# Kernel optimization log

Measured on AMD Instinct MI355X. Metric: run time of the kernel, lower is better.

## Reference

```python
import jax, jax.numpy as jnp
import numpy as np

DIM = 1024
NUM_HEADS = 16
HEAD_DIM = 64
SEQ_LEN = 4096
RMS_EPS = 1e-6


def rotary_tables(T, head_dim):
    # modded-nanogpt style rotary: frequencies only on first half of the half-dim,
    # second half zeroed (identity rotation).
    angular_freq = (1.0 / 1024.0) ** jnp.linspace(0.0, 1.0, head_dim // 4)
    angular_freq = jnp.concatenate([angular_freq, jnp.zeros(head_dim // 4)])
    t = jnp.arange(T, dtype=jnp.float32)
    theta = t[:, None] * angular_freq[None, :]  # [T, D/2]
    return jnp.cos(theta), jnp.sin(theta)


def apply_rotary(x, cos, sin):
    # x: [B, T, H, D]
    xf = x.astype(jnp.float32)
    x1, x2 = jnp.split(xf, 2, axis=-1)
    c = cos[None, :, None, :]
    s = sin[None, :, None, :]
    y1 = x1 * c + x2 * s
    y2 = x1 * (-s) + x2 * c
    return jnp.concatenate([y1, y2], axis=-1).astype(x.dtype)


def rms_norm(x):
    return x * jax.lax.rsqrt(jnp.mean(x * x, axis=-1, keepdims=True) + RMS_EPS)


def setup_inputs() -> dict:
    key = jax.random.key(0)
    k1, k2, k3 = jax.random.split(key, 3)
    hdim = NUM_HEADS * HEAD_DIM
    std = 0.5 * DIM ** (-0.5)
    bound = (3.0 ** 0.5) * std
    x = jax.random.normal(k1, (1, SEQ_LEN, DIM), dtype=jnp.float32)
    qkv_w = jax.random.uniform(k2, (3 * hdim, DIM), minval=-bound, maxval=bound, dtype=jnp.float32)
    # original zero-inits c_proj; use small random weights for a nontrivial baseline
    proj_w = jax.random.normal(k3, (DIM, hdim), dtype=jnp.float32) * 0.02
    lambdas = jnp.array([0.5], dtype=jnp.float32)
    return {"x": x, "qkv_w": qkv_w, "lambdas": lambdas, "proj_w": proj_w}


def reference(x, qkv_w, lambdas, proj_w):
    B, T, _ = x.shape
    H, D = NUM_HEADS, HEAD_DIM
    scale = 1.0 / (D ** 0.5)
    qkv = jnp.einsum('btc,fc->btf', x, qkv_w)            # [B, T, 3*H*D]
    qkv = qkv.reshape(B, T, 3 * H, D)
    q, k, v = jnp.split(qkv, 3, axis=-2)                  # each [B, T, H, D]
    q, k = rms_norm(q), rms_norm(k)
    cos, sin = rotary_tables(T, D)
    q, k = apply_rotary(q, cos, sin), apply_rotary(k, cos, sin)
    v = lambdas[0] * v
    scores = jnp.einsum('bqhd,bkhd->bhqk', q, k) * scale  # [B, H, T, T]
    causal = jnp.tril(jnp.ones((T, T), dtype=bool))
    scores = jnp.where(causal[None, None], scores, -jnp.inf)
    p = jax.nn.softmax(scores, axis=-1)
    y = jnp.einsum('bhqk,bkhd->bqhd', p, v)               # [B, T, H, D]
    y = y.reshape(B, T, H * D)
    return jnp.einsum('btf,cf->btc', y, proj_w)           # [B, T, DIM]
```

## Files before the change

### kernel.cpp

```cpp
#include <hip/hip_runtime.h>
#include <stdint.h>

#define SEQ 4096
#define NHEAD 16
#define HDIM 64

typedef __attribute__((ext_vector_type(4))) float f32x4;
typedef __attribute__((ext_vector_type(16))) float f32x16;
typedef __attribute__((ext_vector_type(8))) __bf16 bf16x8;
typedef __attribute__((ext_vector_type(8))) unsigned short u16x8;
typedef __attribute__((ext_vector_type(4))) unsigned short u16x4;
typedef __attribute__((ext_vector_type(4))) unsigned int u32x4;

static __device__ __forceinline__ float bf2f(unsigned short u) {
    unsigned int x = ((unsigned int)u) << 16;
    return __builtin_bit_cast(float, x);
}
static __device__ __forceinline__ unsigned short f2bf(float f) {
    unsigned int u = __builtin_bit_cast(unsigned int, f);
    u += 0x7FFFu + ((u >> 16) & 1u);
    return (unsigned short)(u >> 16);
}
static __device__ __forceinline__ f32x4 mfma_bf16_16x16x32(u16x8 a, u16x8 b, f32x4 c) {
    return __builtin_amdgcn_mfma_f32_16x16x32_bf16(
        __builtin_bit_cast(bf16x8, a), __builtin_bit_cast(bf16x8, b), c, 0, 0, 0);
}
static __device__ __forceinline__ f32x16 mfma_bf16_32x32x16(u16x8 a, u16x8 b, f32x16 c) {
    return __builtin_amdgcn_mfma_f32_32x32x16_bf16(
        __builtin_bit_cast(bf16x8, a), __builtin_bit_cast(bf16x8, b), c, 0, 0, 0);
}
static __device__ __forceinline__ void gload_lds16(const void* g, void* l) {
    __builtin_amdgcn_global_load_lds(
        (__attribute__((address_space(1))) unsigned int*)g,
        (__attribute__((address_space(3))) unsigned int*)l,
        16, 0, 0);
}
static __device__ __forceinline__ unsigned int cvtpk_bf16(float lo, float hi) {
    unsigned int r;
    asm("v_cvt_pk_bf16_f32 %0, %1, %2" : "=v"(r) : "v"(lo), "v"(hi));
    return r;
}

__global__ void cvt3_kernel(const float* __restrict__ s0, unsigned short* __restrict__ d0, int n0q,
                            const float* __restrict__ s1, unsigned short* __restrict__ d1, int n1q,
                            const float* __restrict__ s2, unsigned short* __restrict__ d2, int n2q)
{
    const int stride = gridDim.x * blockDim.x;
    const int total = n0q + n1q + n2q;
    for (int i = blockIdx.x * blockDim.x + threadIdx.x; i < total; i += stride) {
        const float* src; unsigned short* dst; int j;
        if (i < n0q)            { src = s0; dst = d0; j = i; }
        else if (i < n0q + n1q) { src = s1; dst = d1; j = i - n0q; }
        else                    { src = s2; dst = d2; j = i - n0q - n1q; }
        f32x4 v = *(const f32x4*)(src + (size_t)j * 4);
        u16x4 o;
#pragma unroll
        for (int k = 0; k < 4; k++) o[k] = f2bf(v[k]);
        *(u16x4*)(dst + (size_t)j * 4) = o;
    }
}

template<int OUT_BF16>
__global__ __launch_bounds__(256) void gemm_bt_kernel(
    const unsigned short* __restrict__ A,
    const unsigned short* __restrict__ B,
    void* __restrict__ Cv,
    int M, int N, int K, int lda)
{
    __shared__ __align__(16) unsigned short As[128 * 64];
    __shared__ __align__(16) unsigned short Bs[128 * 64];
    const int tid = threadIdx.x;
    const int lane = tid & 63;
    const int wave = tid >> 6;
    const int wm = (wave >> 1) * 64;
    const int wn = (wave & 1) * 64;
    const int bm = blockIdx.y * 128, bn = blockIdx.x * 128;
    const int l15 = lane & 15, l4 = lane >> 4;

    f32x4 acc[4][4];
#pragma unroll
    for (int i = 0; i < 4; i++)
#pragma unroll
        for (int j = 0; j < 4; j++) acc[i][j] = (f32x4){0.f, 0.f, 0.f, 0.f};

    const int srow = tid >> 3;
    const int scol = (tid & 7) * 8;
    const unsigned short* Ab = A + (size_t)(bm + srow) * lda + scol;
    const unsigned short* Bb = B + (size_t)(bn + srow) * K + scol;

    for (int kt = 0; kt < K; kt += 64) {
#pragma unroll
        for (int ci = 0; ci < 4; ci++)
            gload_lds16(Ab + (size_t)ci * 32 * lda + kt, &As[ci * 2048 + tid * 8]);
#pragma unroll
        for (int ci = 0; ci < 4; ci++)
            gload_lds16(Bb + (size_t)ci * 32 * K + kt, &Bs[ci * 2048 + tid * 8]);
        __syncthreads();
#pragma unroll
        for (int ks = 0; ks < 2; ks++) {
            const int kc = ks * 32 + l4 * 8;
            u16x8 af[4], bfr[4];
#pragma unroll
            for (int i = 0; i < 4; i++)
                af[i] = *(const u16x8*)&As[(wm + i * 16 + l15) * 64 + kc];
#pragma unroll
            for (int j = 0; j < 4; j++)
                bfr[j] = *(const u16x8*)&Bs[(wn + j * 16 + l15) * 64 + kc];
#pragma unroll
            for (int i = 0; i < 4; i++)
#pragma unroll
                for (int j = 0; j < 4; j++)
                    acc[i][j] = mfma_bf16_16x16x32(af[i], bfr[j], acc[i][j]);
        }
        __syncthreads();
    }

    const int orow = bm + wm + l4 * 4;
    const int ocol = bn + wn + l15;
#pragma unroll
    for (int i = 0; i < 4; i++)
#pragma unroll
        for (int j = 0; j < 4; j++)
#pragma unroll
            for (int r = 0; r < 4; r++) {
                size_t idx = (size_t)(orow + i * 16 + r) * N + (ocol + j * 16);
                if (OUT_BF16) ((unsigned short*)Cv)[idx] = f2bf(acc[i][j][r]);
                else          ((float*)Cv)[idx] = acc[i][j][r];
            }
}

__global__ __launch_bounds__(256) void rope_norm_kernel(
    const unsigned short* __restrict__ qkv,
    const float* __restrict__ lambdas,
    unsigned short* __restrict__ qh,
    unsigned short* __restrict__ kh,
    unsigned short* __restrict__ vh)
{
    const int lane = threadIdx.x & 63;
    const int wave = threadIdx.x >> 6;
    const int vec = blockIdx.x * 4 + wave;
    const int t = vec >> 4;
    const int h = vec & 15;
    const size_t base = (size_t)t * 3072 + h * 64 + lane;
    float q = bf2f(qkv[base]);
    float k = bf2f(qkv[base + 1024]);
    float v = bf2f(qkv[base + 2048]);
    float sq = q * q, sk = k * k;
#pragma unroll
    for (int m = 1; m < 64; m <<= 1) {
        sq += __shfl_xor(sq, m);
        sk += __shfl_xor(sk, m);
    }
    q *= rsqrtf(sq * (1.0f / 64.0f) + 1e-6f);
    k *= rsqrtf(sk * (1.0f / 64.0f) + 1e-6f);
    const int i = lane & 31;
    float w = (i < 16) ? exp2f(-(10.0f / 15.0f) * (float)i) : 0.0f;
    float th = (float)t * w;
    float c = cosf(th), s = sinf(th);
    float qp = __shfl_xor(q, 32);
    float kp = __shfl_xor(k, 32);
    float sg = (lane < 32) ? s : -s;
    float qo = (q * c + qp * sg) * 0.1803368801111244f;
    float ko = k * c + kp * sg;
    float vo = v * lambdas[0];
    const size_t o = ((size_t)h * SEQ + t) * 64 + lane;
    qh[o] = f2bf(qo);
    kh[o] = f2bf(ko);
    vh[o] = f2bf(vo);
}

__global__ __launch_bounds__(256) void transpose_v_kernel(
    const unsigned short* __restrict__ vh, unsigned short* __restrict__ vT)
{
    __shared__ __align__(16) unsigned short tile[64][72];
    const int h = blockIdx.x >> 6;
    const int tt = (blockIdx.x & 63) * 64;
    const int tid = threadIdx.x;
    const int row = tid >> 2;
    const int c0 = (tid & 3) * 16;
    const u16x8* src = (const u16x8*)(vh + ((size_t)h * SEQ + tt + row) * 64 + c0);
    u16x8 a = src[0], b = src[1];
#pragma unroll
    for (int j = 0; j < 8; j++) { tile[row][c0 + j] = a[j]; tile[row][c0 + 8 + j] = b[j]; }
    __syncthreads();
    u16x8 o0, o1;
#pragma unroll
    for (int j = 0; j < 8; j++) { o0[j] = tile[c0 + j][row]; o1[j] = tile[c0 + 8 + j][row]; }
    u16x8* dst = (u16x8*)(vT + ((size_t)h * 64 + row) * SEQ + tt + c0);
    dst[0] = o0; dst[1] = o1;
}

__global__ __launch_bounds__(256, 3) void attn_kernel(
    const unsigned short* __restrict__ qh,
    const unsigned short* __restrict__ kh,
    const unsigned short* __restrict__ vT,
    float* __restrict__ acc,
    float* __restrict__ lacc)
{
    __shared__ __align__(16) unsigned short Ks[2][64 * 64];
    __shared__ __align__(16) unsigned short Vs[2][64 * 64];
    const int h = blockIdx.x;
    const int qp = blockIdx.y;
    const int s = blockIdx.z;
    const int tid = threadIdx.x;
    const int lane = tid & 63;
    const int wave = tid >> 6;
    const int l31 = lane & 31;
    const int hi = lane >> 5;
    const int r7 = l31 & 7;

    const unsigned short* Kb = kh + (size_t)h * SEQ * 64;
    const unsigned short* Vb = vT + (size_t)h * 64 * SEQ;

    const int sr = tid >> 3;
    const int scs = ((tid & 7) * 8) ^ ((sr & 7) * 8);

#pragma unroll 1
    for (int ph = 0; ph < 2; ph++) {
        const int qtp = ph ? (31 - qp) : qp;
        const int nt = 2 * qtp + 2;
        const int t0 = (nt * s) / 3;
        const int t1 = (nt * (s + 1)) / 3;
        if (t0 >= t1) continue;
        const int q0w = qtp * 128 + wave * 32;

        u16x8 qf[4];
        {
            const unsigned short* qb = qh + ((size_t)h * SEQ + q0w + l31) * 64 + hi * 8;
#pragma unroll
            for (int c = 0; c < 4; c++) qf[c] = *(const u16x8*)(qb + c * 16);
        }

        f32x16 o0 = {}, o1 = {};
        float l = 0.f;

        {
            const int kv0p = t0 * 64;
            gload_lds16(Kb + (size_t)(kv0p + sr) * 64 + scs,      &Ks[0][tid * 8]);
            gload_lds16(Kb + (size_t)(kv0p + 32 + sr) * 64 + scs, &Ks[0][2048 + tid * 8]);
            gload_lds16(Vb + (size_t)sr * SEQ + kv0p + scs,        &Vs[0][tid * 8]);
            gload_lds16(Vb + (size_t)(32 + sr) * SEQ + kv0p + scs, &Vs[0][2048 + tid * 8]);
        }
        __syncthreads();

        int cur = 0;
        for (int kt = t0; kt < t1; kt++) {
            const int kv0 = kt * 64;
            if (kt + 1 < t1) {
                const int nkv = kv0 + 64;
                gload_lds16(Kb + (size_t)(nkv + sr) * 64 + scs,      &Ks[cur ^ 1][tid * 8]);
                gload_lds16(Kb + (size_t)(nkv + 32 + sr) * 64 + scs, &Ks[cur ^ 1][2048 + tid * 8]);
                gload_lds16(Vb + (size_t)sr * SEQ + nkv + scs,        &Vs[cur ^ 1][tid * 8]);
                gload_lds16(Vb + (size_t)(32 + sr) * SEQ + nkv + scs, &Vs[cur ^ 1][2048 + tid * 8]);
            }
            if (kv0 <= q0w + 31) {
                const unsigned short* ks0 = &Ks[cur][l31 * 64];
                const unsigned short* ks1 = &Ks[cur][(32 + l31) * 64];
                const bool half2 = (kv0 + 32 <= q0w + 31);

                f32x16 st0 = {}, st1 = {};
                __builtin_amdgcn_s_setprio(1);
#pragma unroll
                for (int c = 0; c < 4; c++) {
                    const int off = ((c * 2 + hi) ^ r7) * 8;
                    st0 = mfma_bf16_32x32x16(*(const u16x8*)(ks0 + off), qf[c], st0);
                }
                if (half2) {
#pragma unroll
                    for (int c = 0; c < 4; c++) {
                        const int off = ((c * 2 + hi) ^ r7) * 8;
                        st1 = mfma_bf16_32x32x16(*(const u16x8*)(ks1 + off), qf[c], st1);
                    }
                }
                __builtin_amdgcn_s_setprio(0);

                if (kv0 + 63 > q0w) {
                    const int q = q0w + l31;
#pragma unroll
                    for (int r = 0; r < 16; r++) {
                        const int crow = (r & 3) + 8 * (r >> 2) + 4 * hi;
                        if (kv0 + crow > q)      st0[r] = -1e30f;
                        if (kv0 + 32 + crow > q) st1[r] = -1e30f;
                    }
                }

                float u8[8];
#pragma unroll
                for (int r = 0; r < 16; r++) st0[r] = exp2f(st0[r]);
#pragma unroll
                for (int r = 0; r < 8; r++) u8[r] = st0[r] + st0[r + 8];
                if (half2) {
#pragma unroll
                    for (int r = 0; r < 16; r++) st1[r] = exp2f(st1[r]);
#pragma unroll
                    for (int r = 0; r < 8; r++) u8[r] += st1[r] + st1[r + 8];
                }
#pragma unroll
                for (int r = 0; r < 4; r++) u8[r] += u8[r + 4];
                float ts = (u8[0] + u8[2]) + (u8[1] + u8[3]);
                ts += __shfl_xor(ts, 32);
                l += ts;

                u16x8 paf[4];
#pragma unroll
                for (int kk = 0; kk < 4; kk++) {
                    if (kk >= 2 && !half2) continue;
                    const int rb = (kk & 1) * 8;
                    float p0, p1, p2, p3, p4, p5, p6, p7;
                    if (kk < 2) {
                        p0 = st0[rb + 0]; p1 = st0[rb + 1]; p2 = st0[rb + 2]; p3 = st0[rb + 3];
                        p4 = st0[rb + 4]; p5 = st0[rb + 5]; p6 = st0[rb + 6]; p7 = st0[rb + 7];
                    } else {
                        p0 = st1[rb + 0]; p1 = st1[rb + 1]; p2 = st1[rb + 2]; p3 = st1[rb + 3];
                        p4 = st1[rb + 4]; p5 = st1[rb + 5]; p6 = st1[rb + 6]; p7 = st1[rb + 7];
                    }
                    unsigned int a0 = cvtpk_bf16(p0, p1);
                    unsigned int a1 = cvtpk_bf16(p2, p3);
                    unsigned int b0 = cvtpk_bf16(p4, p5);
                    unsigned int b1 = cvtpk_bf16(p6, p7);
                    asm volatile("v_permlane32_swap_b32 %0, %1" : "+v"(a0), "+v"(b0));
                    asm volatile("v_permlane32_swap_b32 %0, %1" : "+v"(a1), "+v"(b1));
                    u32x4 w;
                    w[0] = a0; w[1] = a1; w[2] = b0; w[3] = b1;
                    paf[kk] = __builtin_bit_cast(u16x8, w);
                }

                const unsigned short* vs0 = &Vs[cur][l31 * 64];
                const unsigned short* vs1 = &Vs[cur][(32 + l31) * 64];
                __builtin_amdgcn_s_setprio(1);
#pragma unroll
                for (int kk = 0; kk < 4; kk++) {
                    if (kk >= 2 && !half2) continue;
                    const int off = ((kk * 2 + hi) ^ r7) * 8;
                    u16x8 v0 = *(const u16x8*)(vs0 + off);
                    u16x8 v1 = *(const u16x8*)(vs1 + off);
                    o0 = mfma_bf16_32x32x16(paf[kk], v0, o0);
                    o1 = mfma_bf16_32x32x16(paf[kk], v1, o1);
                }
                __builtin_amdgcn_s_setprio(0);
            }
            __syncthreads();
            cur ^= 1;
        }

        if (t0 * 64 <= q0w + 31) {
#pragma unroll
            for (int r = 0; r < 16; r++) {
                const int crow = (r & 3) + 8 * (r >> 2) + 4 * hi;
                float* row = acc + (size_t)(q0w + crow) * 1024 + h * 64;
                atomicAdd(row + l31,      o0[r]);
                atomicAdd(row + 32 + l31, o1[r]);
            }
            if (hi == 0) atomicAdd(lacc + (size_t)(q0w + l31) * 16 + h, l);
        }
    }
}

__global__ __launch_bounds__(256) void norm_kernel(
    const float* __restrict__ acc, const float* __restrict__ lacc,
    unsigned short* __restrict__ yb)
{
    const int i = blockIdx.x * 256 + threadIdx.x;
    const int t = i >> 8;
    const int h = (i & 255) >> 4;
    const float inv = 1.0f / lacc[t * 16 + h];
    f32x4 v = *(const f32x4*)(acc + (size_t)i * 4);
    u16x4 o;
#pragma unroll
    for (int j = 0; j < 4; j++) o[j] = f2bf(v[j] * inv);
    *(u16x4*)(yb + (size_t)i * 4) = o;
}

extern "C" void kernel_launch(void* const* d_in, const int* in_sizes, int n_in,
                              void* d_out, int out_size, void* d_ws, size_t ws_size,
                              hipStream_t stream) {
    (void)in_sizes; (void)n_in; (void)out_size; (void)ws_size;
    const float* x       = (const float*)d_in[0];
    const float* qkv_w   = (const float*)d_in[1];
    const float* lambdas = (const float*)d_in[2];
    const float* proj_w  = (const float*)d_in[3];

    char* ws = (char*)d_ws;
    unsigned short* x_bf   = (unsigned short*)(ws + 0);
    unsigned short* qkv_bf = (unsigned short*)(ws + 8388608);
    unsigned short* qh     = (unsigned short*)(ws + 33554432);
    unsigned short* kh     = (unsigned short*)(ws + 41943040);
    unsigned short* vh     = (unsigned short*)(ws + 50331648);
    unsigned short* vT     = (unsigned short*)(ws + 58720256);
    unsigned short* wq_bf  = (unsigned short*)(ws + 67108864);
    unsigned short* wp_bf  = (unsigned short*)(ws + 73400320);
    unsigned short* yb     = (unsigned short*)(ws + 75497472);
    float*          acc    = (float*)(ws + 0);
    float*          lacc   = (float*)(ws + 16777216);

    cvt3_kernel<<<2048, 256, 0, stream>>>(x, x_bf, 1048576,
                                          qkv_w, wq_bf, 786432,
                                          proj_w, wp_bf, 262144);

    gemm_bt_kernel<1><<<dim3(24, 32), 256, 0, stream>>>(x_bf, wq_bf, qkv_bf, 4096, 3072, 1024, 1024);
    rope_norm_kernel<<<16384, 256, 0, stream>>>(qkv_bf, lambdas, qh, kh, vh);
    transpose_v_kernel<<<1024, 256, 0, stream>>>(vh, vT);

    hipMemsetAsync(ws, 0, 16777216 + 262144, stream);

    attn_kernel<<<dim3(16, 16, 3), 256, 0, stream>>>(qh, kh, vT, acc, lacc);
    norm_kernel<<<4096, 256, 0, stream>>>(acc, lacc, yb);

    gemm_bt_kernel<0><<<dim3(8, 32), 256, 0, stream>>>(yb, wp_bf, d_out, 4096, 1024, 1024, 1024);
}
```

Baseline: 192.5 us.

## Load K/V MFMA operands directly from global memory instead of LDS double-buffering

Drops the shared-memory double-buffered K/V staging (async global-to-LDS copies and per-tile __syncthreads) in the attention kernel. Each lane now reads its K and V MFMA fragments straight from global memory through L1/L2. The grid order also changes so that blocks for the same head are launched next to each other, which should improve cache reuse. This removes LDS traffic and barrier stalls, but there is no longer any prefetch, so every wave waits on global-load latency. The four waves of a block also now fetch the same K/V data redundantly.

```diff
diff --git a/kernel.cpp b/kernel.cpp
--- a/kernel.cpp
+++ b/kernel.cpp
@@ -197,23 +197,17 @@
     float* __restrict__ acc,
     float* __restrict__ lacc)
 {
-    __shared__ __align__(16) unsigned short Ks[2][64 * 64];
-    __shared__ __align__(16) unsigned short Vs[2][64 * 64];
-    const int h = blockIdx.x;
-    const int qp = blockIdx.y;
-    const int s = blockIdx.z;
+    const int qp = blockIdx.x;
+    const int s = blockIdx.y;
+    const int h = blockIdx.z;
     const int tid = threadIdx.x;
     const int lane = tid & 63;
     const int wave = tid >> 6;
     const int l31 = lane & 31;
     const int hi = lane >> 5;
-    const int r7 = l31 & 7;
 
     const unsigned short* Kb = kh + (size_t)h * SEQ * 64;
     const unsigned short* Vb = vT + (size_t)h * 64 * SEQ;
-
-    const int sr = tid >> 3;
-    const int scs = ((tid & 7) * 8) ^ ((sr & 7) * 8);
 
 #pragma unroll 1
     for (int ph = 0; ph < 2; ph++) {
@@ -234,43 +228,25 @@
         f32x16 o0 = {}, o1 = {};
         float l = 0.f;
 
-        {
-            const int kv0p = t0 * 64;
-            gload_lds16(Kb + (size_t)(kv0p + sr) * 64 + scs,      &Ks[0][tid * 8]);
-            gload_lds16(Kb + (size_t)(kv0p + 32 + sr) * 64 + scs, &Ks[0][2048 + tid * 8]);
-            gload_lds16(Vb + (size_t)sr * SEQ + kv0p + scs,        &Vs[0][tid * 8]);
-            gload_lds16(Vb + (size_t)(32 + sr) * SEQ + kv0p + scs, &Vs[0][2048 + tid * 8]);
-        }
-        __syncthreads();
-
-        int cur = 0;
+        const unsigned short* Kr0 = Kb + (size_t)(t0 * 64 + l31) * 64 + hi * 8;
+        const unsigned short* Kr1 = Kr0 + 32 * 64;
+        const unsigned short* Vr0 = Vb + (size_t)l31 * SEQ + t0 * 64 + hi * 8;
+        const unsigned short* Vr1 = Vr0 + (size_t)32 * SEQ;
+
         for (int kt = t0; kt < t1; kt++) {
             const int kv0 = kt * 64;
-            if (kt + 1 < t1) {
-                const int nkv = kv0 + 64;
-                gload_lds16(Kb + (size_t)(nkv + sr) * 64 + scs,      &Ks[cur ^ 1][tid * 8]);
-                gload_lds16(Kb + (size_t)(nkv + 32 + sr) * 64 + scs, &Ks[cur ^ 1][2048 + tid * 8]);
-                gload_lds16(Vb + (size_t)sr * SEQ + nkv + scs,        &Vs[cur ^ 1][tid * 8]);
-                gload_lds16(Vb + (size_t)(32 + sr) * SEQ + nkv + scs, &Vs[cur ^ 1][2048 + tid * 8]);
-            }
             if (kv0 <= q0w + 31) {
-                const unsigned short* ks0 = &Ks[cur][l31 * 64];
-                const unsigned short* ks1 = &Ks[cur][(32 + l31) * 64];
                 const bool half2 = (kv0 + 32 <= q0w + 31);
 
                 f32x16 st0 = {}, st1 = {};
                 __builtin_amdgcn_s_setprio(1);
 #pragma unroll
-                for (int c = 0; c < 4; c++) {
-                    const int off = ((c * 2 + hi) ^ r7) * 8;
-                    st0 = mfma_bf16_32x32x16(*(const u16x8*)(ks0 + off), qf[c], st0);
-                }
+                for (int c = 0; c < 4; c++)
+                    st0 = mfma_bf16_32x32x16(*(const u16x8*)(Kr0 + c * 16), qf[c], st0);
                 if (half2) {
 #pragma unroll
-                    for (int c = 0; c < 4; c++) {
-                        const int off = ((c * 2 + hi) ^ r7) * 8;
-                        st1 = mfma_bf16_32x32x16(*(const u16x8*)(ks1 + off), qf[c], st1);
-                    }
+                    for (int c = 0; c < 4; c++)
+                        st1 = mfma_bf16_32x32x16(*(const u16x8*)(Kr1 + c * 16), qf[c], st1);
                 }
                 __builtin_amdgcn_s_setprio(0);
 
@@ -325,22 +301,19 @@
                     paf[kk] = __builtin_bit_cast(u16x8, w);
                 }
 
-                const unsigned short* vs0 = &Vs[cur][l31 * 64];
-                const unsigned short* vs1 = &Vs[cur][(32 + l31) * 64];
                 __builtin_amdgcn_s_setprio(1);
 #pragma unroll
                 for (int kk = 0; kk < 4; kk++) {
                     if (kk >= 2 && !half2) continue;
-                    const int off = ((kk * 2 + hi) ^ r7) * 8;
-                    u16x8 v0 = *(const u16x8*)(vs0 + off);
-                    u16x8 v1 = *(const u16x8*)(vs1 + off);
+                    u16x8 v0 = *(const u16x8*)(Vr0 + kk * 16);
+                    u16x8 v1 = *(const u16x8*)(Vr1 + kk * 16);
                     o0 = mfma_bf16_32x32x16(paf[kk], v0, o0);
                     o1 = mfma_bf16_32x32x16(paf[kk], v1, o1);
                 }
                 __builtin_amdgcn_s_setprio(0);
             }
-            __syncthreads();
-            cur ^= 1;
+            Kr0 += 64 * 64; Kr1 += 64 * 64;
+            Vr0 += 64;      Vr1 += 64;
         }
 
         if (t0 * 64 <= q0w + 31) {
@@ -403,7 +376,7 @@
 
     hipMemsetAsync(ws, 0, 16777216 + 262144, stream);
 
-    attn_kernel<<<dim3(16, 16, 3), 256, 0, stream>>>(qh, kh, vT, acc, lacc);
+    attn_kernel<<<dim3(16, 3, 16), 256, 0, stream>>>(qh, kh, vT, acc, lacc);
     norm_kernel<<<4096, 256, 0, stream>>>(acc, lacc, yb);
 
     gemm_bt_kernel<0><<<dim3(8, 32), 256, 0, stream>>>(yb, wp_bf, d_out, 4096, 1024, 1024, 1024);
```

Result: slower. 257.9 us (+33.9%).
